# Optimization experiments

Measured on AMD Instinct MI355X. Metric: run time of the kernel, lower is better.

## Reference

```python
import jax, jax.numpy as jnp
import numpy as np

N_NODES = 128
N_EDGES = N_NODES * (N_NODES - 1)  # fully-connected, no self-loops
N_IN = 128
N_HID = 256
N_OUT = 128
BATCH = 32


def _build_rel_matrices():
    # one-hot incidence matrices for fully-connected off-diagonal graph
    send_idx, recv_idx = [], []
    for i in range(N_NODES):
        for j in range(N_NODES):
            if i != j:
                send_idx.append(i)
                recv_idx.append(j)
    eye = np.eye(N_NODES, dtype=np.float32)
    rel_send = eye[np.asarray(send_idx)]  # [E, N]
    rel_rec = eye[np.asarray(recv_idx)]   # [E, N]
    return jnp.asarray(rel_rec), jnp.asarray(rel_send)


def setup_inputs() -> dict:
    key = jax.random.key(0)
    k = jax.random.split(key, 6)
    rel_rec, rel_send = _build_rel_matrices()
    s1 = 1.0 / np.sqrt(2 * N_IN)
    s2 = 1.0 / np.sqrt(N_HID)
    return {
        "x": jax.random.normal(k[0], (BATCH, N_NODES, N_IN), dtype=jnp.float32),
        "rel_type": jax.random.uniform(k[1], (BATCH, N_EDGES, 4), dtype=jnp.float32),
        "rel_rec": rel_rec,
        "rel_send": rel_send,
        "W1": jax.random.normal(k[2], (2 * N_IN, N_HID), dtype=jnp.float32) * s1,
        "b1": jnp.zeros((N_HID,), dtype=jnp.float32),
        "W2": jax.random.normal(k[3], (N_HID, N_OUT), dtype=jnp.float32) * s2,
        "b2": jnp.zeros((N_OUT,), dtype=jnp.float32),
    }


def reference(x, rel_type, rel_rec, rel_send, W1, b1, W2, b2):
    # node2edge: gather sender/receiver node features via incidence matmuls
    senders = jnp.einsum('en,bnf->bef', rel_send, x)    # [B, E, n_in]
    receivers = jnp.einsum('en,bnf->bef', rel_rec, x)   # [B, E, n_in]
    edges = jnp.concatenate([senders, receivers], axis=-1)  # [B, E, 2*n_in]
    # 2-layer MLP on edges (rel_type is unused in the original forward)
    h = jax.nn.relu(edges @ W1 + b1)
    msg = h @ W2 + b2                                   # [B, E, n_out]
    # edge2node: scatter-sum then normalize by in-degree
    agg = jnp.einsum('en,bef->bnf', rel_rec, msg)       # [B, N, n_out]
    norm = rel_rec.sum(axis=0)[None, :, None]           # [1, N, 1]
    return agg / (norm + 1e-6)
```

## Files before the change

### kernel.cpp

```cpp
#include <hip/hip_runtime.h>

#define BATCH 32
#define NN    128
#define NIN   128
#define NHID  256
#define NOUT  128
#define ROWS  (BATCH * NN)

__device__ __forceinline__ float4 fma4(float a, const float4 w, const float4 c) {
    float4 r;
    r.x = fmaf(a, w.x, c.x); r.y = fmaf(a, w.y, c.y);
    r.z = fmaf(a, w.z, c.z); r.w = fmaf(a, w.w, c.w);
    return r;
}

__global__ __launch_bounds__(256, 4) void k1_sr(
    const float* __restrict__ x, const float* __restrict__ W1,
    const float* __restrict__ b1, float* __restrict__ S, float* __restrict__ R)
{
    const int t    = threadIdx.x;
    const int c    = (t >> 6) * 64 + (t & 63);
    const int row0 = blockIdx.x * 8;

    float accs[8], accr[8];
#pragma unroll
    for (int r = 0; r < 8; ++r) { accs[r] = 0.f; accr[r] = 0.f; }

    for (int k = 0; k < NIN; k += 4) {
        float wa[4], wb[4];
#pragma unroll
        for (int kk = 0; kk < 4; ++kk) {
            wa[kk] = W1[(size_t)(k + kk) * NHID + c];
            wb[kk] = W1[(size_t)(NIN + k + kk) * NHID + c];
        }
#pragma unroll
        for (int r = 0; r < 8; ++r) {
            const float4 xv = *(const float4*)&x[(size_t)(row0 + r) * NIN + k];
            accs[r] = fmaf(xv.x, wa[0], fmaf(xv.y, wa[1], fmaf(xv.z, wa[2], fmaf(xv.w, wa[3], accs[r]))));
            accr[r] = fmaf(xv.x, wb[0], fmaf(xv.y, wb[1], fmaf(xv.z, wb[2], fmaf(xv.w, wb[3], accr[r]))));
        }
    }
    const float bias = b1[c];
#pragma unroll
    for (int r = 0; r < 8; ++r) {
        S[(size_t)(row0 + r) * NHID + c] = accs[r];
        R[(size_t)(row0 + r) * NHID + c] = accr[r] + bias;
    }
}

__global__ __launch_bounds__(256) void k2_g(
    const float* __restrict__ S, const float* __restrict__ R, float* __restrict__ G)
{
    const int blk = blockIdx.x;
    const int b   = blk >> 3;
    const int cc  = (blk >> 1) & 3;
    const int rh  = blk & 1;

    __shared__ float4 s4[128 * 16];
    const float4* S4 = (const float4*)S;
    const float4* R4 = (const float4*)R;
    float4*       G4 = (float4*)G;
    const int t = threadIdx.x;

    for (int idx = t; idx < 2048; idx += 256)
        s4[idx] = S4[(size_t)(b * NN + (idx >> 4)) * 64 + cc * 16 + (idx & 15)];

    const int cg = t & 15;
    const int n0 = rh * 64 + (t >> 4) * 4;
    float4 rv[4], acc[4];
#pragma unroll
    for (int q = 0; q < 4; ++q) {
        rv[q]  = R4[(size_t)(b * NN + n0 + q) * 64 + cc * 16 + cg];
        acc[q] = make_float4(0.f, 0.f, 0.f, 0.f);
    }
    __syncthreads();

    for (int i = 0; i < 128; ++i) {
        const float4 s = s4[i * 16 + cg];
#pragma unroll
        for (int q = 0; q < 4; ++q) {
            acc[q].x += fmaxf(s.x + rv[q].x, 0.f);
            acc[q].y += fmaxf(s.y + rv[q].y, 0.f);
            acc[q].z += fmaxf(s.z + rv[q].z, 0.f);
            acc[q].w += fmaxf(s.w + rv[q].w, 0.f);
        }
    }
#pragma unroll
    for (int q = 0; q < 4; ++q) {
        const float4 sq = s4[(n0 + q) * 16 + cg];
        acc[q].x -= fmaxf(sq.x + rv[q].x, 0.f);
        acc[q].y -= fmaxf(sq.y + rv[q].y, 0.f);
        acc[q].z -= fmaxf(sq.z + rv[q].z, 0.f);
        acc[q].w -= fmaxf(sq.w + rv[q].w, 0.f);
        G4[(size_t)(b * NN + n0 + q) * 64 + cc * 16 + cg] = acc[q];
    }
}

__global__ __launch_bounds__(256) void k3_out(
    const float* __restrict__ G, const float* __restrict__ W2,
    const float* __restrict__ b2, float* __restrict__ out)
{
    __shared__ float g[16][256];
    const int row0 = blockIdx.x * 16;
    const int t = threadIdx.x;
    const float4* Gg = (const float4*)(G + (size_t)row0 * NHID);
    float4* g4 = (float4*)g;
    for (int idx = t; idx < 1024; idx += 256) g4[idx] = Gg[idx];
    __syncthreads();

    const int c4 = (t & 31) * 4;
    const int r0 = (t >> 5) * 2;
    float4 acc[2];
    acc[0] = make_float4(0.f, 0.f, 0.f, 0.f);
    acc[1] = make_float4(0.f, 0.f, 0.f, 0.f);

    for (int k = 0; k < NHID; k += 4) {
        float4 w[4];
#pragma unroll
        for (int kk = 0; kk < 4; ++kk)
            w[kk] = *(const float4*)&W2[(size_t)(k + kk) * NOUT + c4];
#pragma unroll
        for (int r = 0; r < 2; ++r) {
            const float4 gv = *(const float4*)(&g[r0 + r][k]);
            acc[r] = fma4(gv.x, w[0], fma4(gv.y, w[1], fma4(gv.z, w[2], fma4(gv.w, w[3], acc[r]))));
        }
    }
    const float inv = 1.0f / (127.0f + 1e-6f);
    float4 bias = *(const float4*)&b2[c4];
    bias.x *= 127.f; bias.y *= 127.f; bias.z *= 127.f; bias.w *= 127.f;
#pragma unroll
    for (int r = 0; r < 2; ++r) {
        float4 o;
        o.x = (acc[r].x + bias.x) * inv;
        o.y = (acc[r].y + bias.y) * inv;
        o.z = (acc[r].z + bias.z) * inv;
        o.w = (acc[r].w + bias.w) * inv;
        *(float4*)&out[(size_t)(row0 + r0 + r) * NOUT + c4] = o;
    }
}

extern "C" void kernel_launch(void* const* d_in, const int* in_sizes, int n_in,
                              void* d_out, int out_size, void* d_ws, size_t ws_size,
                              hipStream_t stream)
{
    const float* x  = (const float*)d_in[0];
    const float* W1 = (const float*)d_in[4];
    const float* b1 = (const float*)d_in[5];
    const float* W2 = (const float*)d_in[6];
    const float* b2 = (const float*)d_in[7];
    float* out = (float*)d_out;

    float* S = (float*)d_ws;
    float* R = S + (size_t)ROWS * NHID;
    float* G = R + (size_t)ROWS * NHID;

    k1_sr <<<ROWS / 8,  256, 0, stream>>>(x, W1, b1, S, R);
    k2_g  <<<256,       256, 0, stream>>>(S, R, G);
    k3_out<<<ROWS / 16, 256, 0, stream>>>(G, W2, b2, out);
}
```

Measured before the change: 135.4 us.

## Tile first GEMM through LDS with swizzled x tile and register blocking

Rewrites the first projection kernel as a shared-memory tiled GEMM. Each block stages a 64-row x tile (with an XOR swizzle to avoid bank conflicts) and a 128x64 W1 slab in LDS, then each thread computes a 4x4 output micro-tile using float4 loads. This replaces per-thread global W1 reloads and scalar accumulation with data reuse out of LDS and vectorized stores. It uses 64KB of LDS per block, which limits occupancy (launch bounds drop to 2 blocks).

```diff
diff --git a/kernel.cpp b/kernel.cpp
--- a/kernel.cpp
+++ b/kernel.cpp
@@ -13,38 +13,69 @@
     r.z = fmaf(a, w.z, c.z); r.w = fmaf(a, w.w, c.w);
     return r;
 }
+#define XK(v, kk) ((kk) == 0 ? (v).x : (kk) == 1 ? (v).y : (kk) == 2 ? (v).z : (v).w)
 
-__global__ __launch_bounds__(256, 4) void k1_sr(
+__global__ __launch_bounds__(256, 2) void k1_gemm(
     const float* __restrict__ x, const float* __restrict__ W1,
     const float* __restrict__ b1, float* __restrict__ S, float* __restrict__ R)
 {
-    const int t    = threadIdx.x;
-    const int c    = (t >> 6) * 64 + (t & 63);
-    const int row0 = blockIdx.x * 8;
+    __shared__ float4 xl[64 * 32];
+    __shared__ float4 wl[128 * 16];
 
-    float accs[8], accr[8];
+    const int t  = threadIdx.x;
+    const int ct = blockIdx.x & 7;
+    const int rt = blockIdx.x >> 3;
+    const int h  = ct >> 2;
+    const int c0 = (ct & 3) * 64;
+    const int row0 = rt * 64;
+
+    {
+        const float4* Xg = (const float4*)(x + (size_t)row0 * NIN);
+        for (int idx = t; idx < 2048; idx += 256) {
+            const int row = idx >> 5, jj = idx & 31;
+            xl[row * 32 + (jj ^ (row & 7))] = Xg[idx];
+        }
+    }
+    {
+        const float4* Wg = (const float4*)W1;
+        for (int idx = t; idx < 2048; idx += 256) {
+            const int row = idx >> 4, jj = idx & 15;
+            wl[idx] = Wg[(size_t)(h * 128 + row) * 64 + (c0 >> 2) + jj];
+        }
+    }
+    __syncthreads();
+
+    const int cl = t & 15;
+    const int rg = t >> 4;
+    const int sw = rg & 7;
+
+    float4 acc[4];
 #pragma unroll
-    for (int r = 0; r < 8; ++r) { accs[r] = 0.f; accr[r] = 0.f; }
+    for (int j = 0; j < 4; ++j) acc[j] = make_float4(0.f, 0.f, 0.f, 0.f);
 
-    for (int k = 0; k < NIN; k += 4) {
-        float wa[4], wb[4];
+    for (int k = 0; k < 128; k += 4) {
+        const int kx = (k >> 2) ^ sw;
+        float4 xv[4];
+#pragma unroll
+        for (int j = 0; j < 4; ++j)
+            xv[j] = xl[(rg + 16 * j) * 32 + kx];
 #pragma unroll
         for (int kk = 0; kk < 4; ++kk) {
-            wa[kk] = W1[(size_t)(k + kk) * NHID + c];
-            wb[kk] = W1[(size_t)(NIN + k + kk) * NHID + c];
-        }
+            const float4 w = wl[(k + kk) * 16 + cl];
 #pragma unroll
-        for (int r = 0; r < 8; ++r) {
-            const float4 xv = *(const float4*)&x[(size_t)(row0 + r) * NIN + k];
-            accs[r] = fmaf(xv.x, wa[0], fmaf(xv.y, wa[1], fmaf(xv.z, wa[2], fmaf(xv.w, wa[3], accs[r]))));
-            accr[r] = fmaf(xv.x, wb[0], fmaf(xv.y, wb[1], fmaf(xv.z, wb[2], fmaf(xv.w, wb[3], accr[r]))));
+            for (int j = 0; j < 4; ++j)
+                acc[j] = fma4(XK(xv[j], kk), w, acc[j]);
         }
     }
-    const float bias = b1[c];
+
+    float* dst = h ? R : S;
+    float4 bias = make_float4(0.f, 0.f, 0.f, 0.f);
+    if (h) bias = *(const float4*)&b1[c0 + cl * 4];
 #pragma unroll
-    for (int r = 0; r < 8; ++r) {
-        S[(size_t)(row0 + r) * NHID + c] = accs[r];
-        R[(size_t)(row0 + r) * NHID + c] = accr[r] + bias;
+    for (int j = 0; j < 4; ++j) {
+        float4 v = acc[j];
+        v.x += bias.x; v.y += bias.y; v.z += bias.z; v.w += bias.w;
+        *(float4*)&dst[(size_t)(row0 + rg + 16 * j) * NHID + c0 + cl * 4] = v;
     }
 }
 
@@ -154,7 +185,7 @@
     float* R = S + (size_t)ROWS * NHID;
     float* G = R + (size_t)ROWS * NHID;
 
-    k1_sr <<<ROWS / 8,  256, 0, stream>>>(x, W1, b1, S, R);
-    k2_g  <<<256,       256, 0, stream>>>(S, R, G);
-    k3_out<<<ROWS / 16, 256, 0, stream>>>(G, W2, b2, out);
+    k1_gemm<<<512,       256, 0, stream>>>(x, W1, b1, S, R);
+    k2_g   <<<256,       256, 0, stream>>>(S, R, G);
+    k3_out <<<ROWS / 16, 256, 0, stream>>>(G, W2, b2, out);
 }
```

After: 128.5 us. -5.1%, faster.
